# Performance work log

Hardware: AMD Instinct MI355X
Metric: run time of the kernel (lower is better)

## Reference

```python
import jax, jax.numpy as jnp
import numpy as np

BS, QS, H, NH, HD = 2, 2048, 1024, 16, 64


def setup_inputs() -> dict:
    key = jax.random.key(0)
    ks = jax.random.split(key, 10)
    s = 0.02
    x = jax.random.normal(ks[0], (BS, QS, H), jnp.float32)
    pos_emb = jax.random.normal(ks[1], (QS, H), jnp.float32)
    rr_bias = jax.random.normal(ks[2], (NH, HD), jnp.float32) * s
    rw_bias = jax.random.normal(ks[3], (NH, HD), jnp.float32) * s
    Wq = jax.random.normal(ks[4], (H, NH * HD), jnp.float32) * s
    Wk = jax.random.normal(ks[5], (H, NH * HD), jnp.float32) * s
    Wv = jax.random.normal(ks[6], (H, NH * HD), jnp.float32) * s
    Wr = jax.random.normal(ks[7], (H, NH * HD), jnp.float32) * s
    Wo = jax.random.normal(ks[8], (NH * HD, H), jnp.float32) * s
    ln_gamma = jnp.ones((H,), jnp.float32)
    ln_beta = jnp.zeros((H,), jnp.float32)
    # True = masked (filled with -inf); strict causal mask, ms = ks - qs = 0
    mask = jnp.triu(jnp.ones((QS, QS), bool), 1)
    return {"x": x, "mask": mask, "pos_emb": pos_emb, "rr_bias": rr_bias,
            "rw_bias": rw_bias, "Wq": Wq, "Wk": Wk, "Wv": Wv, "Wr": Wr,
            "Wo": Wo, "ln_gamma": ln_gamma, "ln_beta": ln_beta}


def _left_shift(x, bs):
    # x: [bs, qs, ks, n_head] -- Transformer-XL relative-shift trick
    b, qs, ksz, nh = x.shape
    pad = jnp.zeros((b, qs, 1, nh), x.dtype)
    xp = jnp.concatenate([pad, x], axis=2).reshape(b, ksz + 1, qs, nh)
    x = xp[:, 1:].reshape(b, qs, ksz, nh)
    # NOTE: original code uses diagonal offset (ks - bs) with bs = batch size
    tri = jnp.tril(jnp.ones((qs, ksz), x.dtype), ksz - bs)
    return x * tri[None, :, :, None]


def reference(x, mask, pos_emb, rr_bias, rw_bias, Wq, Wk, Wv, Wr, Wo, ln_gamma, ln_beta):
    bs, qs, hid = x.shape
    nh, dh = rr_bias.shape
    ksz = qs  # self-attention, no memory
    scale = 1.0 / dh ** 0.5
    q = (x @ Wq).reshape(bs, qs, nh, dh)
    k = (x @ Wk).reshape(bs, ksz, nh, dh)
    v = (x @ Wv).reshape(bs, ksz, nh, dh)
    r = (pos_emb @ Wr).reshape(qs, nh, dh)
    AC = jnp.einsum('bqnd,bknd->bqkn', q + rw_bias[None, None], k)
    BD = jnp.einsum('bqnd,knd->bqkn', q + rr_bias[None, None], r)
    BD = _left_shift(BD, bs)
    score = (AC + BD) * scale
    score = jnp.where(mask[None, :, :, None], -jnp.inf, score)
    prob = jax.nn.softmax(score, axis=2)  # softmax over key axis
    att = jnp.einsum('bqkn,bknd->bqnd', prob, v)
    out = att.reshape(bs, qs, nh * dh) @ Wo
    out = x + out  # residual (post-lnorm variant)
    mu = out.mean(-1, keepdims=True)
    var = ((out - mu) ** 2).mean(-1, keepdims=True)
    return (out - mu) / jnp.sqrt(var + 1e-5) * ln_gamma + ln_beta
```

## Files before the change

### kernel.cpp

```cpp
#include <hip/hip_runtime.h>
#include <hip/hip_bf16.h>


typedef _Float16 f16;
typedef __attribute__((ext_vector_type(8))) _Float16 f16x8;
typedef __attribute__((ext_vector_type(4))) float f32x4;

__device__ __forceinline__ void gload16(const f16* g, f16* l) {
  __builtin_amdgcn_global_load_lds((__attribute__((address_space(1))) void*)(g),
                                   (__attribute__((address_space(3))) void*)(l), 16, 0, 0);
}

__global__ __launch_bounds__(256) void cast2_kernel(const float* __restrict__ a,
                                                    f16* __restrict__ ao, int na4,
                                                    const float* __restrict__ b,
                                                    f16* __restrict__ bo, int nb4) {
  int i = blockIdx.x * 256 + threadIdx.x;
  const float* src;
  f16* dst;
  int j;
  if (i < na4) { src = a; dst = ao; j = i; }
  else { j = i - na4; if (j >= nb4) return; src = b; dst = bo; }
  f32x4 v = *(const f32x4*)&src[j * 4];
  f16 o0 = (f16)v[0], o1 = (f16)v[1], o2 = (f16)v[2], o3 = (f16)v[3];
  f16* p = &dst[j * 4];
  p[0] = o0; p[1] = o1; p[2] = o2; p[3] = o3;
}

__global__ __launch_bounds__(256) void wtrans5_kernel(
    const float* __restrict__ W0, const float* __restrict__ W1, const float* __restrict__ W2,
    const float* __restrict__ W3, const float* __restrict__ W4,
    f16* __restrict__ T0, f16* __restrict__ T1, f16* __restrict__ T2,
    f16* __restrict__ T3, f16* __restrict__ T4) {
  __shared__ float tile[32][33];
  const float* W;
  f16* WT;
  switch (blockIdx.z) {
    case 0: W = W0; WT = T0; break;
    case 1: W = W1; WT = T1; break;
    case 2: W = W2; WT = T2; break;
    case 3: W = W3; WT = T3; break;
    default: W = W4; WT = T4; break;
  }
  int k0 = blockIdx.x * 32, n0 = blockIdx.y * 32;
  int tx = threadIdx.x, ty = threadIdx.y;
#pragma unroll
  for (int i = 0; i < 4; ++i)
    tile[ty + i * 8][tx] = W[(size_t)(k0 + ty + i * 8) * 1024 + n0 + tx];
  __syncthreads();
#pragma unroll
  for (int i = 0; i < 4; ++i)
    WT[(size_t)(n0 + ty + i * 8) * 1024 + k0 + tx] = (f16)tile[tx][ty + i * 8];
}

__global__ __launch_bounds__(256) void gemm_qkv(
    const f16* __restrict__ A, const f16* __restrict__ Bq, const f16* __restrict__ Bk,
    const f16* __restrict__ Bv, f16* __restrict__ Qw, f16* __restrict__ Qr,
    f16* __restrict__ Kb, f16* __restrict__ VTb,
    const float* __restrict__ rw, const float* __restrict__ rr) {
  __shared__ f16 sm[17408];
  f16* As = sm;
  f16* Bs = sm + 8192;
  const int bsel = blockIdx.x >> 3;
  const f16* Bw = bsel == 0 ? Bq : (bsel == 1 ? Bk : Bv);
  const int n0 = (blockIdx.x & 7) * 128, m0 = blockIdx.y * 128;
  const int tid = threadIdx.x, lane = tid & 63, wv = tid >> 6;
  const int wm = wv >> 1, wn = wv & 1, lg = lane >> 4, ln = lane & 15;
  const int srow = lane >> 3;
  const int sw = (lane & 7) ^ srow;
  f32x4 acc[4][4] = {};

  for (int kt = 0; kt < 16; ++kt) {
    __syncthreads();
#pragma unroll
    for (int i = 0; i < 4; ++i) {
      int c = wv * 4 + i;
      gload16(A + (size_t)(m0 + c * 8 + srow) * 1024 + kt * 64 + sw * 8, &As[c * 512]);
      gload16(Bw + (size_t)(n0 + c * 8 + srow) * 1024 + kt * 64 + sw * 8, &Bs[c * 512]);
    }
    __syncthreads();
#pragma unroll
    for (int ks = 0; ks < 2; ++ks) {
      f16x8 af[4], bfr[4];
#pragma unroll
      for (int mi = 0; mi < 4; ++mi)
        af[mi] = *(const f16x8*)&As[(wm * 64 + mi * 16 + ln) * 64 +
                                    (((ks * 4 + lg) ^ (ln & 7)) * 8)];
#pragma unroll
      for (int ni = 0; ni < 4; ++ni)
        bfr[ni] = *(const f16x8*)&Bs[(wn * 64 + ni * 16 + ln) * 64 +
                                     (((ks * 4 + lg) ^ (ln & 7)) * 8)];
#pragma unroll
      for (int mi = 0; mi < 4; ++mi)
#pragma unroll
        for (int ni = 0; ni < 4; ++ni)
          acc[mi][ni] = __builtin_amdgcn_mfma_f32_16x16x32_f16(af[mi], bfr[ni],
                                                               acc[mi][ni], 0, 0, 0);
    }
  }

  if (bsel == 2) {
    __syncthreads();
    f16* T = sm;
#pragma unroll
    for (int mi = 0; mi < 4; ++mi)
#pragma unroll
      for (int ni = 0; ni < 4; ++ni)
#pragma unroll
        for (int r = 0; r < 4; ++r) {
          int ml = wm * 64 + mi * 16 + 4 * lg + r;
          int cl = wn * 64 + ni * 16 + ln;
          T[cl * 136 + ml] = (f16)acc[mi][ni][r];
        }
    __syncthreads();
    int cl = tid >> 1, mb = (tid & 1) * 64;
    int gc = n0 + cl, gm = m0 + mb;
    int hh = gc >> 6, dd = gc & 63, bb = gm >> 11, ss = gm & 2047;
    f16* dst = VTb + ((size_t)(bb * 16 + hh) * 64 + dd) * 2048 + ss;
    const f16* srcT = &T[cl * 136 + mb];
#pragma unroll
    for (int i = 0; i < 8; ++i) *(f16x8*)&dst[i * 8] = *(const f16x8*)&srcT[i * 8];
  } else {
#pragma unroll
    for (int mi = 0; mi < 4; ++mi)
#pragma unroll
      for (int ni = 0; ni < 4; ++ni)
#pragma unroll
        for (int r = 0; r < 4; ++r) {
          int m = m0 + wm * 64 + mi * 16 + 4 * lg + r;
          int c = n0 + wn * 64 + ni * 16 + ln;
          float v = acc[mi][ni][r];
          size_t off = (size_t)m * 1024 + c;
          if (bsel == 0) {
            Qw[off] = (f16)(v + rw[c]);
            Qr[off] = (f16)(v + rr[c]);
          } else {
            Kb[off] = (f16)v;
          }
        }
  }
}

template <int MODE>
__global__ __launch_bounds__(256) void gemm64(
    const f16* __restrict__ A, const f16* __restrict__ Bw,
    f16* __restrict__ out0, float* __restrict__ fout, const float* __restrict__ xres) {
  __shared__ f16 As[4096];
  __shared__ f16 Bs[8192];
  const int tid = threadIdx.x, lane = tid & 63, wv = tid >> 6;
  const int wm = wv >> 1, wn = wv & 1, lg = lane >> 4, ln = lane & 15;
  const int m0 = blockIdx.y * 64, n0 = blockIdx.x * 128;
  const int srow = lane >> 3;
  const int sw = (lane & 7) ^ srow;
  f32x4 acc[2][4] = {};

  for (int kt = 0; kt < 16; ++kt) {
    __syncthreads();
#pragma unroll
    for (int i = 0; i < 2; ++i) {
      int c = wv * 2 + i;
      gload16(A + (size_t)(m0 + c * 8 + srow) * 1024 + kt * 64 + sw * 8, &As[c * 512]);
    }
#pragma unroll
    for (int i = 0; i < 4; ++i) {
      int c = wv * 4 + i;
      gload16(Bw + (size_t)(n0 + c * 8 + srow) * 1024 + kt * 64 + sw * 8, &Bs[c * 512]);
    }
    __syncthreads();
#pragma unroll
    for (int ks = 0; ks < 2; ++ks) {
      f16x8 af[2], bfr[4];
#pragma unroll
      for (int mi = 0; mi < 2; ++mi)
        af[mi] = *(const f16x8*)&As[(wm * 32 + mi * 16 + ln) * 64 +
                                    (((ks * 4 + lg) ^ (ln & 7)) * 8)];
#pragma unroll
      for (int ni = 0; ni < 4; ++ni)
        bfr[ni] = *(const f16x8*)&Bs[(wn * 64 + ni * 16 + ln) * 64 +
                                     (((ks * 4 + lg) ^ (ln & 7)) * 8)];
#pragma unroll
      for (int mi = 0; mi < 2; ++mi)
#pragma unroll
        for (int ni = 0; ni < 4; ++ni)
          acc[mi][ni] = __builtin_amdgcn_mfma_f32_16x16x32_f16(af[mi], bfr[ni],
                                                               acc[mi][ni], 0, 0, 0);
    }
  }
#pragma unroll
  for (int mi = 0; mi < 2; ++mi)
#pragma unroll
    for (int ni = 0; ni < 4; ++ni)
#pragma unroll
      for (int r = 0; r < 4; ++r) {
        int m = m0 + wm * 32 + mi * 16 + 4 * lg + r;
        int c = n0 + wn * 64 + ni * 16 + ln;
        size_t off = (size_t)m * 1024 + c;
        if (MODE == 3) out0[off] = (f16)acc[mi][ni][r];
        else fout[off] = acc[mi][ni][r] + xres[off];
      }
}

__device__ __forceinline__ void chunk_map(int c, int& qt, int& ci) {
  if (c < 8) { qt = c; ci = 0; }
  else if (c < 24) { qt = 8 + ((c - 8) >> 1); ci = (c - 8) & 1; }
  else if (c < 48) { int d = c - 24; qt = 16 + d / 3; ci = d % 3; }
  else { int d = c - 48; qt = 24 + (d >> 2); ci = d & 3; }
}

__global__ __launch_bounds__(256) void attn_chunk(
    const f16* __restrict__ Qw, const f16* __restrict__ Qr,
    const f16* __restrict__ Kb, const f16* __restrict__ VT,
    const f16* __restrict__ Rb, f16* __restrict__ attb,
    f16* __restrict__ Opart, float* __restrict__ Mlp) {
  constexpr int LD = 72;
  constexpr int MW = 88;
  __shared__ f16 Kl[64 * LD];
  __shared__ f16 Vl[64 * LD];
  __shared__ f16 Rl[128 * LD];
  __shared__ f16 Sl[64 * MW];

  int qt, ci;
  chunk_map(blockIdx.x, qt, ci);
  const int h = blockIdx.y, b = blockIdx.z;
  const int q0 = qt * 64;
  const int kts = ci * 8;
  const int kte = min(kts + 7, qt);
  const int tid = threadIdx.x, lane = tid & 63, wv = tid >> 6;
  const int lg = lane >> 4, ln = lane & 15;

  const size_t qoff = ((size_t)(b * 2048 + q0 + wv * 16 + ln) * 16 + h) * 64 + 8 * lg;
  f16x8 aqw[2], aqr[2];
  aqw[0] = *(const f16x8*)&Qw[qoff];
  aqw[1] = *(const f16x8*)&Qw[qoff + 32];
  aqr[0] = *(const f16x8*)&Qr[qoff];
  aqr[1] = *(const f16x8*)&Qr[qoff + 32];

  f32x4 oacc[4] = {};
  float mrun[4] = {-1e30f, -1e30f, -1e30f, -1e30f};
  float lrun[4] = {0.f, 0.f, 0.f, 0.f};

  const int r4 = tid >> 2, c16 = (tid & 3) * 16;
  const int t0 = 48 - 16 * wv;

  f16x8 pk[2], pv[2], prn[2];
  auto load_kv = [&](int kt) {
    const int k0 = kt * 64;
    const f16* ksrc = Kb + ((size_t)(b * 2048 + k0 + r4) * 16 + h) * 64 + c16;
    pk[0] = *(const f16x8*)&ksrc[0];
    pk[1] = *(const f16x8*)&ksrc[8];
    const f16* vsrc = VT + ((size_t)(b * 16 + h) * 64 + r4) * 2048 + k0 + c16;
    pv[0] = *(const f16x8*)&vsrc[0];
    pv[1] = *(const f16x8*)&vsrc[8];
  };
  auto load_r = [&](int jbcur) {
    const int j = jbcur + 128 + r4;
    if (j < 2048) {
      const f16* rsrc = Rb + ((size_t)j * 16 + h) * 64 + c16;
      prn[0] = *(const f16x8*)&rsrc[0];
      prn[1] = *(const f16x8*)&rsrc[8];
    } else {
      f16x8 z = {};
      prn[0] = z;
      prn[1] = z;
    }
  };
  auto write_kv = [&]() {
    *(f16x8*)&Kl[r4 * LD + c16] = pk[0];
    *(f16x8*)&Kl[r4 * LD + c16 + 8] = pk[1];
    *(f16x8*)&Vl[r4 * LD + c16] = pv[0];
    *(f16x8*)&Vl[r4 * LD + c16 + 8] = pv[1];
  };
  auto write_r = [&](int jbcur) {
    const int slot = (jbcur + r4) & 127;
    *(f16x8*)&Rl[slot * LD + c16] = prn[0];
    *(f16x8*)&Rl[slot * LD + c16 + 8] = prn[1];
  };

  const int jb0 = 1984 - q0 + kts * 64;
  load_kv(kts);
  write_kv();
  {
    const int r2 = tid >> 1, c32 = (tid & 1) * 32;
    const int j = jb0 + r2;
    const int slot = j & 127;
    if (j < 2048) {
      const f16* rsrc = Rb + ((size_t)j * 16 + h) * 64 + c32;
#pragma unroll
      for (int i = 0; i < 4; ++i)
        *(f16x8*)&Rl[slot * LD + c32 + i * 8] = *(const f16x8*)&rsrc[i * 8];
    } else {
      f16x8 z = {};
#pragma unroll
      for (int i = 0; i < 4; ++i) *(f16x8*)&Rl[slot * LD + c32 + i * 8] = z;
    }
  }
  __syncthreads();

  for (int kt = kts; kt <= kte; ++kt) {
    const int k0 = kt * 64;
    const int jb = 1984 - q0 + k0;
    if (kt < kte) {
      load_kv(kt + 1);
      load_r(jb);
    }

    f32x4 sc[4] = {};
#pragma unroll
    for (int ks = 0; ks < 2; ++ks)
#pragma unroll
      for (int ni = 0; ni < 4; ++ni) {
        f16x8 kf = *(const f16x8*)&Kl[(ni * 16 + ln) * LD + ks * 32 + 8 * lg];
        sc[ni] = __builtin_amdgcn_mfma_f32_16x16x32_f16(aqw[ks], kf, sc[ni], 0, 0, 0);
      }

    f32x4 mw[5] = {};
#pragma unroll
    for (int ks = 0; ks < 2; ++ks)
#pragma unroll
      for (int nj = 0; nj < 5; ++nj) {
        const int slot = (jb + t0 + nj * 16 + ln) & 127;
        f16x8 rf = *(const f16x8*)&Rl[slot * LD + ks * 32 + 8 * lg];
        mw[nj] = __builtin_amdgcn_mfma_f32_16x16x32_f16(aqr[ks], rf, mw[nj], 0, 0, 0);
      }

#pragma unroll
    for (int nj = 0; nj < 5; ++nj)
#pragma unroll
      for (int r = 0; r < 4; ++r)
        Sl[(wv * 16 + 4 * lg + r) * MW + nj * 16 + ln] = (f16)mw[nj][r];

#pragma unroll
    for (int ni = 0; ni < 4; ++ni)
#pragma unroll
      for (int r = 0; r < 4; ++r) {
        int ql = 4 * lg + r;
        int ki = ni * 16 + ln;
        float bd = (float)Sl[(wv * 16 + ql) * MW + ki - ql + 15];
        float s = (sc[ni][r] + bd) * 0.125f;
        if (k0 + ki > q0 + wv * 16 + ql) s = -1e30f;
        sc[ni][r] = s;
      }

#pragma unroll
    for (int r = 0; r < 4; ++r) {
      float mx = sc[0][r];
#pragma unroll
      for (int ni = 1; ni < 4; ++ni) mx = fmaxf(mx, sc[ni][r]);
#pragma unroll
      for (int off = 1; off < 16; off <<= 1) mx = fmaxf(mx, __shfl_xor(mx, off, 16));
      float mnew = fmaxf(mrun[r], mx);
      float corr = __expf(mrun[r] - mnew);
      mrun[r] = mnew;
      float rs = 0.f;
#pragma unroll
      for (int ni = 0; ni < 4; ++ni) {
        float p = __expf(sc[ni][r] - mnew);
        sc[ni][r] = p;
        rs += p;
      }
#pragma unroll
      for (int off = 1; off < 16; off <<= 1) rs += __shfl_xor(rs, off, 16);
      lrun[r] = lrun[r] * corr + rs;
#pragma unroll
      for (int ni = 0; ni < 4; ++ni) oacc[ni][r] *= corr;
    }

#pragma unroll
    for (int ni = 0; ni < 4; ++ni)
#pragma unroll
      for (int r = 0; r < 4; ++r)
        Sl[(wv * 16 + 4 * lg + r) * MW + ni * 16 + ln] = (f16)sc[ni][r];

#pragma unroll
    for (int ks = 0; ks < 2; ++ks) {
      f16x8 pf = *(const f16x8*)&Sl[(wv * 16 + ln) * MW + ks * 32 + 8 * lg];
#pragma unroll
      for (int ni = 0; ni < 4; ++ni) {
        f16x8 vf = *(const f16x8*)&Vl[(ni * 16 + ln) * LD + ks * 32 + 8 * lg];
        oacc[ni] = __builtin_amdgcn_mfma_f32_16x16x32_f16(pf, vf, oacc[ni], 0, 0, 0);
      }
    }

    __syncthreads();
    if (kt < kte) {
      write_kv();
      write_r(jb);
      __syncthreads();
    }
  }

  if (qt < 8) {
#pragma unroll
    for (int ni = 0; ni < 4; ++ni)
#pragma unroll
      for (int r = 0; r < 4; ++r)
        Sl[(wv * 16 + 4 * lg + r) * MW + ni * 16 + ln] = (f16)(oacc[ni][r] / lrun[r]);
#pragma unroll
    for (int i = 0; i < 2; ++i) {
      int row = wv * 16 + i * 8 + (lane >> 3);
      int col = (lane & 7) * 8;
      *(f16x8*)&attb[((size_t)(b * 2048 + q0 + row) * 16 + h) * 64 + col] =
          *(const f16x8*)&Sl[row * MW + col];
    }
  } else {
    const size_t pidx = (size_t)(b * 16 + h) * 80 + blockIdx.x;
#pragma unroll
    for (int ni = 0; ni < 4; ++ni)
#pragma unroll
      for (int r = 0; r < 4; ++r)
        Sl[(wv * 16 + 4 * lg + r) * MW + ni * 16 + ln] = (f16)oacc[ni][r];
    if (ln == 0) {
#pragma unroll
      for (int r = 0; r < 4; ++r) {
        int row = wv * 16 + 4 * lg + r;
        Mlp[pidx * 128 + row] = mrun[r];
        Mlp[pidx * 128 + 64 + row] = lrun[r];
      }
    }
#pragma unroll
    for (int i = 0; i < 2; ++i) {
      int row = wv * 16 + i * 8 + (lane >> 3);
      int col = (lane & 7) * 8;
      *(f16x8*)&Opart[pidx * 4096 + row * 64 + col] = *(const f16x8*)&Sl[row * MW + col];
    }
  }
}

__global__ __launch_bounds__(256) void combine_kernel(
    const f16* __restrict__ Opart, const float* __restrict__ Mlp,
    f16* __restrict__ attb) {
  const int qt = 8 + blockIdx.x, h = blockIdx.y, b = blockIdx.z;
  const int nc = (qt + 8) >> 3;
  int cbase;
  if (qt < 16) cbase = 8 + 2 * (qt - 8);
  else if (qt < 24) cbase = 24 + 3 * (qt - 16);
  else cbase = 48 + 4 * (qt - 24);
  const int tid = threadIdx.x;
  const int row = tid >> 2, d0 = (tid & 3) * 16;
  const size_t pbase = (size_t)(b * 16 + h) * 80 + cbase;

  float m[4], l[4], w[4];
  float M = -1e30f;
#pragma unroll
  for (int i = 0; i < 4; ++i)
    if (i < nc) {
      m[i] = Mlp[(pbase + i) * 128 + row];
      l[i] = Mlp[(pbase + i) * 128 + 64 + row];
      M = fmaxf(M, m[i]);
    }
  float wsum = 0.f;
#pragma unroll
  for (int i = 0; i < 4; ++i)
    if (i < nc) {
      w[i] = __expf(m[i] - M);
      wsum += w[i] * l[i];
    }
  float o[16] = {};
#pragma unroll
  for (int i = 0; i < 4; ++i)
    if (i < nc) {
      const f16* src = &Opart[(pbase + i) * 4096 + row * 64 + d0];
      f16x8 v0 = *(const f16x8*)&src[0];
      f16x8 v1 = *(const f16x8*)&src[8];
#pragma unroll
      for (int j = 0; j < 8; ++j) {
        o[j] += w[i] * (float)v0[j];
        o[8 + j] += w[i] * (float)v1[j];
      }
    }
  float inv = 1.f / wsum;
  f16x8 r0, r1;
#pragma unroll
  for (int j = 0; j < 8; ++j) {
    r0[j] = (f16)(o[j] * inv);
    r1[j] = (f16)(o[8 + j] * inv);
  }
  f16* dst = &attb[((size_t)(b * 2048 + qt * 64 + row) * 16 + h) * 64 + d0];
  *(f16x8*)&dst[0] = r0;
  *(f16x8*)&dst[8] = r1;
}

__global__ __launch_bounds__(256) void ln_kernel(const float* __restrict__ pre,
                                                 const float* __restrict__ gamma,
                                                 const float* __restrict__ beta,
                                                 float* __restrict__ out) {
  __shared__ float red[8];
  const int row = blockIdx.x, t = threadIdx.x;
  f32x4 v = *(const f32x4*)&pre[(size_t)row * 1024 + t * 4];
  float s = v[0] + v[1] + v[2] + v[3];
  float s2 = v[0] * v[0] + v[1] * v[1] + v[2] * v[2] + v[3] * v[3];
#pragma unroll
  for (int off = 1; off < 64; off <<= 1) {
    s += __shfl_xor(s, off, 64);
    s2 += __shfl_xor(s2, off, 64);
  }
  if ((t & 63) == 0) {
    red[t >> 6] = s;
    red[(t >> 6) + 4] = s2;
  }
  __syncthreads();
  s = red[0] + red[1] + red[2] + red[3];
  s2 = red[4] + red[5] + red[6] + red[7];
  float mean = s * (1.f / 1024.f);
  float var = s2 * (1.f / 1024.f) - mean * mean;
  float rcp = rsqrtf(var + 1e-5f);
  f32x4 g = *(const f32x4*)&gamma[t * 4];
  f32x4 be = *(const f32x4*)&beta[t * 4];
  f32x4 o;
#pragma unroll
  for (int j = 0; j < 4; ++j) o[j] = (v[j] - mean) * rcp * g[j] + be[j];
  *(f32x4*)&out[(size_t)row * 1024 + t * 4] = o;
}

extern "C" void kernel_launch(void* const* d_in, const int* in_sizes, int n_in,
                              void* d_out, int out_size, void* d_ws, size_t ws_size,
                              hipStream_t stream) {
  const float* x = (const float*)d_in[0];
  const float* pe = (const float*)d_in[2];
  const float* rr = (const float*)d_in[3];
  const float* rw = (const float*)d_in[4];
  const float* Wq = (const float*)d_in[5];
  const float* Wk = (const float*)d_in[6];
  const float* Wv = (const float*)d_in[7];
  const float* Wr = (const float*)d_in[8];
  const float* Wo = (const float*)d_in[9];
  const float* gamma = (const float*)d_in[10];
  const float* beta = (const float*)d_in[11];
  float* out = (float*)d_out;

  char* w = (char*)d_ws;
  auto alloc = [&](size_t bytes) {
    char* p = w;
    w += (bytes + 255) & ~(size_t)255;
    return p;
  };
  float* preln = (float*)alloc(4096ull * 1024 * 4);
  f16* xb = (f16*)alloc(4096ull * 1024 * 2);
  f16* pb = (f16*)alloc(2048ull * 1024 * 2);
  f16* WTq = (f16*)alloc(1024ull * 1024 * 2);
  f16* WTk = (f16*)alloc(1024ull * 1024 * 2);
  f16* WTv = (f16*)alloc(1024ull * 1024 * 2);
  f16* WTr = (f16*)alloc(1024ull * 1024 * 2);
  f16* WTo = (f16*)alloc(1024ull * 1024 * 2);
  f16* Qw = (f16*)alloc(4096ull * 1024 * 2);
  f16* Qr = (f16*)alloc(4096ull * 1024 * 2);
  f16* Kb = (f16*)alloc(4096ull * 1024 * 2);
  f16* VTb = (f16*)alloc(4096ull * 1024 * 2);
  f16* Rb = (f16*)alloc(2048ull * 1024 * 2);
  f16* attb = (f16*)alloc(4096ull * 1024 * 2);
  f16* Opart = (f16*)alloc(2ull * 16 * 80 * 4096 * 2);
  float* Mlp = (float*)alloc(2ull * 16 * 80 * 128 * 4);

  cast2_kernel<<<6144, 256, 0, stream>>>(x, xb, 4096 * 1024 / 4, pe, pb, 2048 * 1024 / 4);
  wtrans5_kernel<<<dim3(32, 32, 5), dim3(32, 8), 0, stream>>>(Wq, Wk, Wv, Wr, Wo,
                                                              WTq, WTk, WTv, WTr, WTo);

  gemm_qkv<<<dim3(24, 32), 256, 0, stream>>>(xb, WTq, WTk, WTv, Qw, Qr, Kb, VTb, rw, rr);
  gemm64<3><<<dim3(8, 32), 256, 0, stream>>>(pb, WTr, Rb, nullptr, nullptr);

  attn_chunk<<<dim3(80, 16, 2), 256, 0, stream>>>(Qw, Qr, Kb, VTb, Rb, attb, Opart, Mlp);
  combine_kernel<<<dim3(24, 16, 2), 256, 0, stream>>>(Opart, Mlp, attb);

  gemm64<4><<<dim3(8, 64), 256, 0, stream>>>(attb, WTo, nullptr, preln, x);
  ln_kernel<<<4096, 256, 0, stream>>>(preln, gamma, beta, out);
}
```

Baseline: 320.1 us.

## Merge R projection into QKV GEMM and enlarge attention query tile

Folds the positional R projection into the QKV GEMM launch as a fourth weight group, which removes a separate kernel launch. The attention kernel now uses 128-row query tiles with 512 threads, so K/V tiles are shared across twice as many query rows, and it launches the heaviest chunks first through a reversed block index. The R ring buffer, partial-output buffers and combine kernel are resized for the new tile shape. The trade-off is more LDS per block and fewer blocks, which can lower occupancy and load balance.

```diff
diff --git a/kernel.cpp b/kernel.cpp
--- a/kernel.cpp
+++ b/kernel.cpp
@@ -53,16 +53,20 @@
     WT[(size_t)(n0 + ty + i * 8) * 1024 + k0 + tx] = (f16)tile[tx][ty + i * 8];
 }
 
-__global__ __launch_bounds__(256) void gemm_qkv(
-    const f16* __restrict__ A, const f16* __restrict__ Bq, const f16* __restrict__ Bk,
-    const f16* __restrict__ Bv, f16* __restrict__ Qw, f16* __restrict__ Qr,
-    f16* __restrict__ Kb, f16* __restrict__ VTb,
+__global__ __launch_bounds__(256) void gemm_qkvr(
+    const f16* __restrict__ A, const f16* __restrict__ pb,
+    const f16* __restrict__ Bq, const f16* __restrict__ Bk,
+    const f16* __restrict__ Bv, const f16* __restrict__ Br,
+    f16* __restrict__ Qw, f16* __restrict__ Qr,
+    f16* __restrict__ Kb, f16* __restrict__ VTb, f16* __restrict__ Rb,
     const float* __restrict__ rw, const float* __restrict__ rr) {
   __shared__ f16 sm[17408];
   f16* As = sm;
   f16* Bs = sm + 8192;
   const int bsel = blockIdx.x >> 3;
-  const f16* Bw = bsel == 0 ? Bq : (bsel == 1 ? Bk : Bv);
+  if (bsel == 3 && blockIdx.y >= 16) return;
+  const f16* Ap = (bsel == 3) ? pb : A;
+  const f16* Bw = bsel == 0 ? Bq : (bsel == 1 ? Bk : (bsel == 2 ? Bv : Br));
   const int n0 = (blockIdx.x & 7) * 128, m0 = blockIdx.y * 128;
   const int tid = threadIdx.x, lane = tid & 63, wv = tid >> 6;
   const int wm = wv >> 1, wn = wv & 1, lg = lane >> 4, ln = lane & 15;
@@ -75,7 +79,7 @@
 #pragma unroll
     for (int i = 0; i < 4; ++i) {
       int c = wv * 4 + i;
-      gload16(A + (size_t)(m0 + c * 8 + srow) * 1024 + kt * 64 + sw * 8, &As[c * 512]);
+      gload16(Ap + (size_t)(m0 + c * 8 + srow) * 1024 + kt * 64 + sw * 8, &As[c * 512]);
       gload16(Bw + (size_t)(n0 + c * 8 + srow) * 1024 + kt * 64 + sw * 8, &Bs[c * 512]);
     }
     __syncthreads();
@@ -134,17 +138,18 @@
           if (bsel == 0) {
             Qw[off] = (f16)(v + rw[c]);
             Qr[off] = (f16)(v + rr[c]);
+          } else if (bsel == 1) {
+            Kb[off] = (f16)v;
           } else {
-            Kb[off] = (f16)v;
+            Rb[off] = (f16)v;
           }
         }
   }
 }
 
-template <int MODE>
-__global__ __launch_bounds__(256) void gemm64(
+__global__ __launch_bounds__(256) void gemm_o(
     const f16* __restrict__ A, const f16* __restrict__ Bw,
-    f16* __restrict__ out0, float* __restrict__ fout, const float* __restrict__ xres) {
+    float* __restrict__ fout, const float* __restrict__ xres) {
   __shared__ f16 As[4096];
   __shared__ f16 Bs[8192];
   const int tid = threadIdx.x, lane = tid & 63, wv = tid >> 6;
@@ -195,19 +200,18 @@
         int m = m0 + wm * 32 + mi * 16 + 4 * lg + r;
         int c = n0 + wn * 64 + ni * 16 + ln;
         size_t off = (size_t)m * 1024 + c;
-        if (MODE == 3) out0[off] = (f16)acc[mi][ni][r];
-        else fout[off] = acc[mi][ni][r] + xres[off];
+        fout[off] = acc[mi][ni][r] + xres[off];
       }
 }
 
 __device__ __forceinline__ void chunk_map(int c, int& qt, int& ci) {
-  if (c < 8) { qt = c; ci = 0; }
-  else if (c < 24) { qt = 8 + ((c - 8) >> 1); ci = (c - 8) & 1; }
-  else if (c < 48) { int d = c - 24; qt = 16 + d / 3; ci = d % 3; }
-  else { int d = c - 48; qt = 24 + (d >> 2); ci = d & 3; }
-}
-
-__global__ __launch_bounds__(256) void attn_chunk(
+  if (c < 4) { qt = c; ci = 0; }
+  else if (c < 12) { qt = 4 + ((c - 4) >> 1); ci = (c - 4) & 1; }
+  else if (c < 24) { int d = c - 12; qt = 8 + d / 3; ci = d % 3; }
+  else { int d = c - 24; qt = 12 + (d >> 2); ci = d & 3; }
+}
+
+__global__ __launch_bounds__(512) void attn_chunk(
     const f16* __restrict__ Qw, const f16* __restrict__ Qr,
     const f16* __restrict__ Kb, const f16* __restrict__ VT,
     const f16* __restrict__ Rb, f16* __restrict__ attb,
@@ -216,15 +220,16 @@
   constexpr int MW = 88;
   __shared__ f16 Kl[64 * LD];
   __shared__ f16 Vl[64 * LD];
-  __shared__ f16 Rl[128 * LD];
-  __shared__ f16 Sl[64 * MW];
+  __shared__ f16 Rl[256 * LD];
+  __shared__ f16 Sl[128 * MW];
 
   int qt, ci;
-  chunk_map(blockIdx.x, qt, ci);
+  chunk_map(39 - blockIdx.x, qt, ci);
+  const int c = 39 - blockIdx.x;
   const int h = blockIdx.y, b = blockIdx.z;
-  const int q0 = qt * 64;
+  const int q0 = qt * 128;
   const int kts = ci * 8;
-  const int kte = min(kts + 7, qt);
+  const int kte = min(kts + 7, 2 * qt + 1);
   const int tid = threadIdx.x, lane = tid & 63, wv = tid >> 6;
   const int lg = lane >> 4, ln = lane & 15;
 
@@ -239,66 +244,46 @@
   float mrun[4] = {-1e30f, -1e30f, -1e30f, -1e30f};
   float lrun[4] = {0.f, 0.f, 0.f, 0.f};
 
-  const int r4 = tid >> 2, c16 = (tid & 3) * 16;
-  const int t0 = 48 - 16 * wv;
-
-  f16x8 pk[2], pv[2], prn[2];
+  const int r8 = tid >> 3, c8 = (tid & 7) * 8;
+  const int t0w = 112 - 16 * wv;
+
+  f16x8 pk, pv, prn;
   auto load_kv = [&](int kt) {
     const int k0 = kt * 64;
-    const f16* ksrc = Kb + ((size_t)(b * 2048 + k0 + r4) * 16 + h) * 64 + c16;
-    pk[0] = *(const f16x8*)&ksrc[0];
-    pk[1] = *(const f16x8*)&ksrc[8];
-    const f16* vsrc = VT + ((size_t)(b * 16 + h) * 64 + r4) * 2048 + k0 + c16;
-    pv[0] = *(const f16x8*)&vsrc[0];
-    pv[1] = *(const f16x8*)&vsrc[8];
+    pk = *(const f16x8*)&Kb[((size_t)(b * 2048 + k0 + r8) * 16 + h) * 64 + c8];
+    pv = *(const f16x8*)&VT[((size_t)(b * 16 + h) * 64 + r8) * 2048 + k0 + c8];
   };
   auto load_r = [&](int jbcur) {
-    const int j = jbcur + 128 + r4;
-    if (j < 2048) {
-      const f16* rsrc = Rb + ((size_t)j * 16 + h) * 64 + c16;
-      prn[0] = *(const f16x8*)&rsrc[0];
-      prn[1] = *(const f16x8*)&rsrc[8];
-    } else {
-      f16x8 z = {};
-      prn[0] = z;
-      prn[1] = z;
-    }
+    const int j = jbcur + 191 + r8;
+    if (j < 2048) prn = *(const f16x8*)&Rb[((size_t)j * 16 + h) * 64 + c8];
+    else { f16x8 z = {}; prn = z; }
   };
   auto write_kv = [&]() {
-    *(f16x8*)&Kl[r4 * LD + c16] = pk[0];
-    *(f16x8*)&Kl[r4 * LD + c16 + 8] = pk[1];
-    *(f16x8*)&Vl[r4 * LD + c16] = pv[0];
-    *(f16x8*)&Vl[r4 * LD + c16 + 8] = pv[1];
+    *(f16x8*)&Kl[r8 * LD + c8] = pk;
+    *(f16x8*)&Vl[r8 * LD + c8] = pv;
   };
   auto write_r = [&](int jbcur) {
-    const int slot = (jbcur + r4) & 127;
-    *(f16x8*)&Rl[slot * LD + c16] = prn[0];
-    *(f16x8*)&Rl[slot * LD + c16 + 8] = prn[1];
+    const int slot = (jbcur + 191 + r8) & 255;
+    *(f16x8*)&Rl[slot * LD + c8] = prn;
   };
 
-  const int jb0 = 1984 - q0 + kts * 64;
+  const int jb0 = 1920 - q0 + kts * 64;
   load_kv(kts);
   write_kv();
-  {
-    const int r2 = tid >> 1, c32 = (tid & 1) * 32;
-    const int j = jb0 + r2;
-    const int slot = j & 127;
-    if (j < 2048) {
-      const f16* rsrc = Rb + ((size_t)j * 16 + h) * 64 + c32;
-#pragma unroll
-      for (int i = 0; i < 4; ++i)
-        *(f16x8*)&Rl[slot * LD + c32 + i * 8] = *(const f16x8*)&rsrc[i * 8];
-    } else {
-      f16x8 z = {};
-#pragma unroll
-      for (int i = 0; i < 4; ++i) *(f16x8*)&Rl[slot * LD + c32 + i * 8] = z;
-    }
+#pragma unroll
+  for (int pass = 0; pass < 3; ++pass) {
+    const int t = pass * 64 + r8;
+    const int j = jb0 + t;
+    const int slot = j & 255;
+    if (j < 2048)
+      *(f16x8*)&Rl[slot * LD + c8] = *(const f16x8*)&Rb[((size_t)j * 16 + h) * 64 + c8];
+    else { f16x8 z = {}; *(f16x8*)&Rl[slot * LD + c8] = z; }
   }
   __syncthreads();
 
   for (int kt = kts; kt <= kte; ++kt) {
     const int k0 = kt * 64;
-    const int jb = 1984 - q0 + k0;
+    const int jb = 1920 - q0 + k0;
     if (kt < kte) {
       load_kv(kt + 1);
       load_r(jb);
@@ -318,7 +303,7 @@
     for (int ks = 0; ks < 2; ++ks)
 #pragma unroll
       for (int nj = 0; nj < 5; ++nj) {
-        const int slot = (jb + t0 + nj * 16 + ln) & 127;
+        const int slot = (jb + t0w + nj * 16 + ln) & 255;
         f16x8 rf = *(const f16x8*)&Rl[slot * LD + ks * 32 + 8 * lg];
         mw[nj] = __builtin_amdgcn_mfma_f32_16x16x32_f16(aqr[ks], rf, mw[nj], 0, 0, 0);
       }
@@ -389,7 +374,7 @@
     }
   }
 
-  if (qt < 8) {
+  if (qt < 4) {
 #pragma unroll
     for (int ni = 0; ni < 4; ++ni)
 #pragma unroll
@@ -403,7 +388,7 @@
           *(const f16x8*)&Sl[row * MW + col];
     }
   } else {
-    const size_t pidx = (size_t)(b * 16 + h) * 80 + blockIdx.x;
+    const size_t pidx = (size_t)(b * 16 + h) * 40 + c;
 #pragma unroll
     for (int ni = 0; ni < 4; ++ni)
 #pragma unroll
@@ -413,15 +398,15 @@
 #pragma unroll
       for (int r = 0; r < 4; ++r) {
         int row = wv * 16 + 4 * lg + r;
-        Mlp[pidx * 128 + row] = mrun[r];
-        Mlp[pidx * 128 + 64 + row] = lrun[r];
+        Mlp[pidx * 256 + row] = mrun[r];
+        Mlp[pidx * 256 + 128 + row] = lrun[r];
       }
     }
 #pragma unroll
     for (int i = 0; i < 2; ++i) {
       int row = wv * 16 + i * 8 + (lane >> 3);
       int col = (lane & 7) * 8;
-      *(f16x8*)&Opart[pidx * 4096 + row * 64 + col] = *(const f16x8*)&Sl[row * MW + col];
+      *(f16x8*)&Opart[pidx * 8192 + row * 64 + col] = *(const f16x8*)&Sl[row * MW + col];
     }
   }
 }
@@ -429,55 +414,59 @@
 __global__ __launch_bounds__(256) void combine_kernel(
     const f16* __restrict__ Opart, const float* __restrict__ Mlp,
     f16* __restrict__ attb) {
-  const int qt = 8 + blockIdx.x, h = blockIdx.y, b = blockIdx.z;
-  const int nc = (qt + 8) >> 3;
+  const int qt = 4 + blockIdx.x, h = blockIdx.y, b = blockIdx.z;
+  const int nc = (2 * qt + 9) >> 3;
   int cbase;
-  if (qt < 16) cbase = 8 + 2 * (qt - 8);
-  else if (qt < 24) cbase = 24 + 3 * (qt - 16);
-  else cbase = 48 + 4 * (qt - 24);
+  if (qt < 8) cbase = 4 + 2 * (qt - 4);
+  else if (qt < 12) cbase = 12 + 3 * (qt - 8);
+  else cbase = 24 + 4 * (qt - 12);
   const int tid = threadIdx.x;
-  const int row = tid >> 2, d0 = (tid & 3) * 16;
-  const size_t pbase = (size_t)(b * 16 + h) * 80 + cbase;
-
-  float m[4], l[4], w[4];
-  float M = -1e30f;
-#pragma unroll
-  for (int i = 0; i < 4; ++i)
-    if (i < nc) {
-      m[i] = Mlp[(pbase + i) * 128 + row];
-      l[i] = Mlp[(pbase + i) * 128 + 64 + row];
-      M = fmaxf(M, m[i]);
-    }
-  float wsum = 0.f;
-#pragma unroll
-  for (int i = 0; i < 4; ++i)
-    if (i < nc) {
-      w[i] = __expf(m[i] - M);
-      wsum += w[i] * l[i];
-    }
-  float o[16] = {};
-#pragma unroll
-  for (int i = 0; i < 4; ++i)
-    if (i < nc) {
-      const f16* src = &Opart[(pbase + i) * 4096 + row * 64 + d0];
-      f16x8 v0 = *(const f16x8*)&src[0];
-      f16x8 v1 = *(const f16x8*)&src[8];
-#pragma unroll
-      for (int j = 0; j < 8; ++j) {
-        o[j] += w[i] * (float)v0[j];
-        o[8 + j] += w[i] * (float)v1[j];
-      }
-    }
-  float inv = 1.f / wsum;
-  f16x8 r0, r1;
-#pragma unroll
-  for (int j = 0; j < 8; ++j) {
-    r0[j] = (f16)(o[j] * inv);
-    r1[j] = (f16)(o[8 + j] * inv);
-  }
-  f16* dst = &attb[((size_t)(b * 2048 + qt * 64 + row) * 16 + h) * 64 + d0];
-  *(f16x8*)&dst[0] = r0;
-  *(f16x8*)&dst[8] = r1;
+  const size_t pbase = (size_t)(b * 16 + h) * 40 + cbase;
+
+#pragma unroll
+  for (int half = 0; half < 2; ++half) {
+    const int row = half * 64 + (tid >> 2);
+    const int d0 = (tid & 3) * 16;
+    float m[4], l[4], w[4];
+    float M = -1e30f;
+#pragma unroll
+    for (int i = 0; i < 4; ++i)
+      if (i < nc) {
+        m[i] = Mlp[(pbase + i) * 256 + row];
+        l[i] = Mlp[(pbase + i) * 256 + 128 + row];
+        M = fmaxf(M, m[i]);
+      }
+    float wsum = 0.f;
+#pragma unroll
+    for (int i = 0; i < 4; ++i)
+      if (i < nc) {
+        w[i] = __expf(m[i] - M);
+        wsum += w[i] * l[i];
+      }
+    float o[16] = {};
+#pragma unroll
+    for (int i = 0; i < 4; ++i)
+      if (i < nc) {
+        const f16* src = &Opart[(pbase + i) * 8192 + row * 64 + d0];
+        f16x8 v0 = *(const f16x8*)&src[0];
+        f16x8 v1 = *(const f16x8*)&src[8];
+#pragma unroll
+        for (int j = 0; j < 8; ++j) {
+          o[j] += w[i] * (float)v0[j];
+          o[8 + j] += w[i] * (float)v1[j];
+        }
+      }
+    float inv = 1.f / wsum;
+    f16x8 r0, r1;
+#pragma unroll
+    for (int j = 0; j < 8; ++j) {
+      r0[j] = (f16)(o[j] * inv);
+      r1[j] = (f16)(o[8 + j] * inv);
+    }
+    f16* dst = &attb[((size_t)(b * 2048 + qt * 128 + row) * 16 + h) * 64 + d0];
+    *(f16x8*)&dst[0] = r0;
+    *(f16x8*)&dst[8] = r1;
+  }
 }
 
 __global__ __launch_bounds__(256) void ln_kernel(const float* __restrict__ pre,
@@ -548,19 +537,19 @@
   f16* VTb = (f16*)alloc(4096ull * 1024 * 2);
   f16* Rb = (f16*)alloc(2048ull * 1024 * 2);
   f16* attb = (f16*)alloc(4096ull * 1024 * 2);
-  f16* Opart = (f16*)alloc(2ull * 16 * 80 * 4096 * 2);
-  float* Mlp = (float*)alloc(2ull * 16 * 80 * 128 * 4);
+  f16* Opart = (f16*)alloc(2ull * 16 * 40 * 8192 * 2);
+  float* Mlp = (float*)alloc(2ull * 16 * 40 * 256 * 4);
 
   cast2_kernel<<<6144, 256, 0, stream>>>(x, xb, 4096 * 1024 / 4, pe, pb, 2048 * 1024 / 4);
   wtrans5_kernel<<<dim3(32, 32, 5), dim3(32, 8), 0, stream>>>(Wq, Wk, Wv, Wr, Wo,
                                                               WTq, WTk, WTv, WTr, WTo);
 
-  gemm_qkv<<<dim3(24, 32), 256, 0, stream>>>(xb, WTq, WTk, WTv, Qw, Qr, Kb, VTb, rw, rr);
-  gemm64<3><<<dim3(8, 32), 256, 0, stream>>>(pb, WTr, Rb, nullptr, nullptr);
-
-  attn_chunk<<<dim3(80, 16, 2), 256, 0, stream>>>(Qw, Qr, Kb, VTb, Rb, attb, Opart, Mlp);
-  combine_kernel<<<dim3(24, 16, 2), 256, 0, stream>>>(Opart, Mlp, attb);
-
-  gemm64<4><<<dim3(8, 64), 256, 0, stream>>>(attb, WTo, nullptr, preln, x);
+  gemm_qkvr<<<dim3(32, 32), 256, 0, stream>>>(xb, pb, WTq, WTk, WTv, WTr,
+                                              Qw, Qr, Kb, VTb, Rb, rw, rr);
+
+  attn_chunk<<<dim3(40, 16, 2), 512, 0, stream>>>(Qw, Qr, Kb, VTb, Rb, attb, Opart, Mlp);
+  combine_kernel<<<dim3(12, 16, 2), 256, 0, stream>>>(Opart, Mlp, attb);
+
+  gemm_o<<<dim3(8, 64), 256, 0, stream>>>(attb, WTo, preln, x);
   ln_kernel<<<4096, 256, 0, stream>>>(preln, gamma, beta, out);
 }
```

Result: slower. 336.9 us (+5.3%).

## Merge prep kernels and R projection into QKV GEMM, reorder attention blocks

Applied to the files above, without the earlier changes.

Folds the fp32-to-fp16 casts and the five weight transposes into one prep kernel, and folds the positional R projection into the QKV GEMM launch as a fourth weight group with 128-row tiles. Block indices in the GEMMs are remapped so that neighbouring blocks on different XCDs share A/B tiles. The attention chunk order is reversed so the heaviest causal query tiles are scheduled first. Together these cut launch count and tail imbalance, at the cost of more branching inside kernels and extra index arithmetic.

```diff
diff --git a/kernel.cpp b/kernel.cpp
--- a/kernel.cpp
+++ b/kernel.cpp
@@ -11,59 +11,73 @@
                                    (__attribute__((address_space(3))) void*)(l), 16, 0, 0);
 }
 
-__global__ __launch_bounds__(256) void cast2_kernel(const float* __restrict__ a,
-                                                    f16* __restrict__ ao, int na4,
-                                                    const float* __restrict__ b,
-                                                    f16* __restrict__ bo, int nb4) {
-  int i = blockIdx.x * 256 + threadIdx.x;
-  const float* src;
-  f16* dst;
-  int j;
-  if (i < na4) { src = a; dst = ao; j = i; }
-  else { j = i - na4; if (j >= nb4) return; src = b; dst = bo; }
-  f32x4 v = *(const f32x4*)&src[j * 4];
-  f16 o0 = (f16)v[0], o1 = (f16)v[1], o2 = (f16)v[2], o3 = (f16)v[3];
-  f16* p = &dst[j * 4];
-  p[0] = o0; p[1] = o1; p[2] = o2; p[3] = o3;
-}
-
-__global__ __launch_bounds__(256) void wtrans5_kernel(
-    const float* __restrict__ W0, const float* __restrict__ W1, const float* __restrict__ W2,
-    const float* __restrict__ W3, const float* __restrict__ W4,
+__global__ __launch_bounds__(256) void prep_kernel(
+    const float* __restrict__ x, f16* __restrict__ xb,
+    const float* __restrict__ pe, f16* __restrict__ pb,
+    const float* __restrict__ W0, const float* __restrict__ W1,
+    const float* __restrict__ W2, const float* __restrict__ W3,
+    const float* __restrict__ W4,
     f16* __restrict__ T0, f16* __restrict__ T1, f16* __restrict__ T2,
     f16* __restrict__ T3, f16* __restrict__ T4) {
   __shared__ float tile[32][33];
-  const float* W;
-  f16* WT;
-  switch (blockIdx.z) {
-    case 0: W = W0; WT = T0; break;
-    case 1: W = W1; WT = T1; break;
-    case 2: W = W2; WT = T2; break;
-    case 3: W = W3; WT = T3; break;
-    default: W = W4; WT = T4; break;
-  }
-  int k0 = blockIdx.x * 32, n0 = blockIdx.y * 32;
-  int tx = threadIdx.x, ty = threadIdx.y;
-#pragma unroll
-  for (int i = 0; i < 4; ++i)
-    tile[ty + i * 8][tx] = W[(size_t)(k0 + ty + i * 8) * 1024 + n0 + tx];
-  __syncthreads();
-#pragma unroll
-  for (int i = 0; i < 4; ++i)
-    WT[(size_t)(n0 + ty + i * 8) * 1024 + k0 + tx] = (f16)tile[tx][ty + i * 8];
-}
-
-__global__ __launch_bounds__(256) void gemm_qkv(
-    const f16* __restrict__ A, const f16* __restrict__ Bq, const f16* __restrict__ Bk,
-    const f16* __restrict__ Bv, f16* __restrict__ Qw, f16* __restrict__ Qr,
-    f16* __restrict__ Kb, f16* __restrict__ VTb,
+  const int id = blockIdx.x, tid = threadIdx.x;
+  if (id < 6144) {
+    int i = id * 256 + tid;
+    const float* src;
+    f16* dst;
+    int j;
+    if (i < 1048576) { src = x; dst = xb; j = i; }
+    else { j = i - 1048576; src = pe; dst = pb; }
+    f32x4 v = *(const f32x4*)&src[(size_t)j * 4];
+    f16* p = &dst[(size_t)j * 4];
+    p[0] = (f16)v[0]; p[1] = (f16)v[1]; p[2] = (f16)v[2]; p[3] = (f16)v[3];
+  } else {
+    const int wid = id - 6144;
+    const int wsel = wid >> 10, rem = wid & 1023;
+    const float* W;
+    f16* WT;
+    switch (wsel) {
+      case 0: W = W0; WT = T0; break;
+      case 1: W = W1; WT = T1; break;
+      case 2: W = W2; WT = T2; break;
+      case 3: W = W3; WT = T3; break;
+      default: W = W4; WT = T4; break;
+    }
+    const int k0 = (rem >> 5) * 32, n0 = (rem & 31) * 32;
+    const int tx = tid & 31, ty = tid >> 5;
+#pragma unroll
+    for (int i = 0; i < 4; ++i)
+      tile[ty + i * 8][tx] = W[(size_t)(k0 + ty + i * 8) * 1024 + n0 + tx];
+    __syncthreads();
+#pragma unroll
+    for (int i = 0; i < 4; ++i)
+      WT[(size_t)(n0 + ty + i * 8) * 1024 + k0 + tx] = (f16)tile[tx][ty + i * 8];
+  }
+}
+
+__global__ __launch_bounds__(256) void gemm_qkvr(
+    const f16* __restrict__ A, const f16* __restrict__ pb,
+    const f16* __restrict__ Bq, const f16* __restrict__ Bk,
+    const f16* __restrict__ Bv, const f16* __restrict__ Br,
+    f16* __restrict__ Qw, f16* __restrict__ Qr,
+    f16* __restrict__ Kb, f16* __restrict__ VTb, f16* __restrict__ Rb,
     const float* __restrict__ rw, const float* __restrict__ rr) {
   __shared__ f16 sm[17408];
   f16* As = sm;
   f16* Bs = sm + 8192;
-  const int bsel = blockIdx.x >> 3;
-  const f16* Bw = bsel == 0 ? Bq : (bsel == 1 ? Bk : Bv);
-  const int n0 = (blockIdx.x & 7) * 128, m0 = blockIdx.y * 128;
+  const int id2 = (blockIdx.x & 7) * 112 + (blockIdx.x >> 3);
+  int bsel, n0, m0;
+  if (id2 < 768) {
+    bsel = id2 >> 8;
+    n0 = (id2 & 7) * 128;
+    m0 = ((id2 & 255) >> 3) * 128;
+  } else {
+    bsel = 3;
+    n0 = ((id2 - 768) & 7) * 128;
+    m0 = ((id2 - 768) >> 3) * 128;
+  }
+  const f16* Ap = (bsel == 3) ? pb : A;
+  const f16* Bw = bsel == 0 ? Bq : (bsel == 1 ? Bk : (bsel == 2 ? Bv : Br));
   const int tid = threadIdx.x, lane = tid & 63, wv = tid >> 6;
   const int wm = wv >> 1, wn = wv & 1, lg = lane >> 4, ln = lane & 15;
   const int srow = lane >> 3;
@@ -75,7 +89,7 @@
 #pragma unroll
     for (int i = 0; i < 4; ++i) {
       int c = wv * 4 + i;
-      gload16(A + (size_t)(m0 + c * 8 + srow) * 1024 + kt * 64 + sw * 8, &As[c * 512]);
+      gload16(Ap + (size_t)(m0 + c * 8 + srow) * 1024 + kt * 64 + sw * 8, &As[c * 512]);
       gload16(Bw + (size_t)(n0 + c * 8 + srow) * 1024 + kt * 64 + sw * 8, &Bs[c * 512]);
     }
     __syncthreads();
@@ -134,22 +148,24 @@
           if (bsel == 0) {
             Qw[off] = (f16)(v + rw[c]);
             Qr[off] = (f16)(v + rr[c]);
+          } else if (bsel == 1) {
+            Kb[off] = (f16)v;
           } else {
-            Kb[off] = (f16)v;
+            Rb[off] = (f16)v;
           }
         }
   }
 }
 
-template <int MODE>
-__global__ __launch_bounds__(256) void gemm64(
+__global__ __launch_bounds__(256) void gemm_o(
     const f16* __restrict__ A, const f16* __restrict__ Bw,
-    f16* __restrict__ out0, float* __restrict__ fout, const float* __restrict__ xres) {
+    float* __restrict__ fout, const float* __restrict__ xres) {
   __shared__ f16 As[4096];
   __shared__ f16 Bs[8192];
+  const int id2 = (blockIdx.x & 7) * 64 + (blockIdx.x >> 3);
+  const int n0 = (id2 & 7) * 128, m0 = (id2 >> 3) * 64;
   const int tid = threadIdx.x, lane = tid & 63, wv = tid >> 6;
   const int wm = wv >> 1, wn = wv & 1, lg = lane >> 4, ln = lane & 15;
-  const int m0 = blockIdx.y * 64, n0 = blockIdx.x * 128;
   const int srow = lane >> 3;
   const int sw = (lane & 7) ^ srow;
   f32x4 acc[2][4] = {};
@@ -195,8 +211,7 @@
         int m = m0 + wm * 32 + mi * 16 + 4 * lg + r;
         int c = n0 + wn * 64 + ni * 16 + ln;
         size_t off = (size_t)m * 1024 + c;
-        if (MODE == 3) out0[off] = (f16)acc[mi][ni][r];
-        else fout[off] = acc[mi][ni][r] + xres[off];
+        fout[off] = acc[mi][ni][r] + xres[off];
       }
 }
 
@@ -219,8 +234,9 @@
   __shared__ f16 Rl[128 * LD];
   __shared__ f16 Sl[64 * MW];
 
+  const int c = 79 - blockIdx.x;
   int qt, ci;
-  chunk_map(blockIdx.x, qt, ci);
+  chunk_map(c, qt, ci);
   const int h = blockIdx.y, b = blockIdx.z;
   const int q0 = qt * 64;
   const int kts = ci * 8;
@@ -403,7 +419,7 @@
           *(const f16x8*)&Sl[row * MW + col];
     }
   } else {
-    const size_t pidx = (size_t)(b * 16 + h) * 80 + blockIdx.x;
+    const size_t pidx = (size_t)(b * 16 + h) * 80 + c;
 #pragma unroll
     for (int ni = 0; ni < 4; ++ni)
 #pragma unroll
@@ -551,16 +567,15 @@
   f16* Opart = (f16*)alloc(2ull * 16 * 80 * 4096 * 2);
   float* Mlp = (float*)alloc(2ull * 16 * 80 * 128 * 4);
 
-  cast2_kernel<<<6144, 256, 0, stream>>>(x, xb, 4096 * 1024 / 4, pe, pb, 2048 * 1024 / 4);
-  wtrans5_kernel<<<dim3(32, 32, 5), dim3(32, 8), 0, stream>>>(Wq, Wk, Wv, Wr, Wo,
-                                                              WTq, WTk, WTv, WTr, WTo);
-
-  gemm_qkv<<<dim3(24, 32), 256, 0, stream>>>(xb, WTq, WTk, WTv, Qw, Qr, Kb, VTb, rw, rr);
-  gemm64<3><<<dim3(8, 32), 256, 0, stream>>>(pb, WTr, Rb, nullptr, nullptr);
+  prep_kernel<<<11264, 256, 0, stream>>>(x, xb, pe, pb, Wq, Wk, Wv, Wr, Wo,
+                                         WTq, WTk, WTv, WTr, WTo);
+
+  gemm_qkvr<<<896, 256, 0, stream>>>(xb, pb, WTq, WTk, WTv, WTr,
+                                     Qw, Qr, Kb, VTb, Rb, rw, rr);
 
   attn_chunk<<<dim3(80, 16, 2), 256, 0, stream>>>(Qw, Qr, Kb, VTb, Rb, attb, Opart, Mlp);
   combine_kernel<<<dim3(24, 16, 2), 256, 0, stream>>>(Opart, Mlp, attb);
 
-  gemm64<4><<<dim3(8, 64), 256, 0, stream>>>(attb, WTo, nullptr, preln, x);
+  gemm_o<<<512, 256, 0, stream>>>(attb, WTo, preln, x);
   ln_kernel<<<4096, 256, 0, stream>>>(preln, gamma, beta, out);
 }
```

After: 313.8 us. 1.02x faster.
